# Optimization experiments

Measured on AMD Instinct MI355X. Metric: run time of the kernel, lower is better.

## Reference

```python
import jax, jax.numpy as jnp
from jax import lax
import numpy as np

B, H, Wd, CIN, COUT, KH, KW = 64, 64, 64, 128, 256, 3, 3
WSTD, BSTD = 0.3, 0.3
DN = ('NHWC', 'HWIO', 'NHWC')


def setup_inputs() -> dict:
    key = jax.random.key(0)
    k1, k2, k3, k4, k5 = jax.random.split(key, 5)
    X = jax.random.normal(k1, (B, H, Wd, CIN), dtype=jnp.float32)
    W = jax.random.normal(k2, (KH, KW, CIN, COUT), dtype=jnp.float32) * 0.05
    bias = jax.random.normal(k3, (COUT,), dtype=jnp.float32) * 0.05
    # per-sample multiplicative noise: |1 + N(0, std)| as in the original layer
    Werr = jnp.abs(1.0 + WSTD * jax.random.normal(k4, (B, KH, KW, CIN, COUT), dtype=jnp.float32))
    Berr = jnp.abs(1.0 + BSTD * jax.random.normal(k5, (B, COUT), dtype=jnp.float32))
    return {"X": X, "W": W, "bias": bias, "Werr": Werr, "Berr": Berr}


def _conv_single(x, w):
    # x: [H, W, Cin], w: [kh, kw, Cin, Cout] -> [Ho, Wo, Cout], VALID, stride 1
    return lax.conv_general_dilated(x[None], w, window_strides=(1, 1),
                                    padding='VALID', dimension_numbers=DN)[0]


def reference(X, W, bias, Werr, Berr):
    # per-sample noisy filters: memW[b] = W * Werr[b]
    memW = W[None] * Werr                        # [B, kh, kw, Cin, Cout]
    Z = jax.vmap(_conv_single)(X, memW)          # [B, Ho, Wo, Cout]
    membias = bias[None] * Berr                  # [B, Cout]
    return Z + membias[:, None, None, :]
```

## Files before the change

kernel.cpp:

```cpp
#include <hip/hip_runtime.h>
#include <hip/hip_bf16.h>

#define NB   64
#define NH   64
#define NW   64
#define NCI  128
#define NCO  256
#define NHO  62
#define NWO  62
#define MTOT (NHO*NWO)
#define KTOT (9*NCI)

#define BM  256
#define BN  256
#define BK  64
#define NKT (KTOT/BK)
#define MT  16

using bf16x8 = __attribute__((ext_vector_type(8))) short;
using f32x4  = __attribute__((ext_vector_type(4))) float;

__device__ __forceinline__ void gload_lds16(const __hip_bfloat16* g,
                                            __hip_bfloat16* l) {
    __builtin_amdgcn_global_load_lds(
        (const __attribute__((address_space(1))) unsigned int*)g,
        (__attribute__((address_space(3))) unsigned int*)l,
        16, 0, 0);
}

#define SBAR()   __builtin_amdgcn_s_barrier()
#define SCHED()  __builtin_amdgcn_sched_barrier(0)
#define VMCNT(n) asm volatile("s_waitcnt vmcnt(" #n ")" ::: "memory")

__global__ __launch_bounds__(256)
void cvt_x_kernel(const float* __restrict__ X,
                  __hip_bfloat16* __restrict__ Xb, int n8) {
    int i = blockIdx.x * 256 + threadIdx.x;
    if (i >= n8) return;
    const float4* p = (const float4*)X + (size_t)i * 2;
    float4 a = p[0], c = p[1];
    union { __hip_bfloat16 h[8]; float4 v; } u;
    u.h[0] = __float2bfloat16(a.x); u.h[1] = __float2bfloat16(a.y);
    u.h[2] = __float2bfloat16(a.z); u.h[3] = __float2bfloat16(a.w);
    u.h[4] = __float2bfloat16(c.x); u.h[5] = __float2bfloat16(c.y);
    u.h[6] = __float2bfloat16(c.z); u.h[7] = __float2bfloat16(c.w);
    *((float4*)Xb + i) = u.v;
}

#define TK 64
#define TN 64
#define TPAD 65
__global__ __launch_bounds__(256)
void build_wt_kernel(const float* __restrict__ W,
                     const float* __restrict__ Werr,
                     __hip_bfloat16* __restrict__ Wt) {
    __shared__ __hip_bfloat16 tile[TK * TPAD];
    const int t  = threadIdx.x;
    const int b  = blockIdx.z;
    const int k0 = blockIdx.x * TK;
    const int n0 = blockIdx.y * TN;

    const int c4 = (t & 15) * 4;
    const int r  = t >> 4;
    const float* wb = W + n0;
    const float* eb = Werr + (size_t)b * (KTOT * NCO) + n0;
#pragma unroll
    for (int p = 0; p < 4; p++) {
        int k  = k0 + r + p * 16;
        int kl = r + p * 16;
        float4 w = *(const float4*)(wb + (size_t)k * NCO + c4);
        float4 e = *(const float4*)(eb + (size_t)k * NCO + c4);
        tile[kl * TPAD + c4 + 0] = __float2bfloat16(w.x * e.x);
        tile[kl * TPAD + c4 + 1] = __float2bfloat16(w.y * e.y);
        tile[kl * TPAD + c4 + 2] = __float2bfloat16(w.z * e.z);
        tile[kl * TPAD + c4 + 3] = __float2bfloat16(w.w * e.w);
    }
    __syncthreads();
    const int np = t >> 2;
    const int ks = (t & 3) * 16;
    __hip_bfloat16* ob = Wt + ((size_t)b * NCO + n0 + np) * KTOT + k0 + ks;
    union { __hip_bfloat16 h[8]; float4 v; } u;
#pragma unroll
    for (int h2 = 0; h2 < 2; h2++) {
#pragma unroll
        for (int q = 0; q < 8; q++) u.h[q] = tile[(ks + h2 * 8 + q) * TPAD + np];
        *(float4*)(ob + h2 * 8) = u.v;
    }
}

__global__ __launch_bounds__(512, 2)
void gemm_bf16_kernel(const __hip_bfloat16* __restrict__ Xb,
                      const __hip_bfloat16* __restrict__ Wt,
                      const float* __restrict__ bias,
                      const float* __restrict__ Berr,
                      float* __restrict__ out) {
    __shared__ __hip_bfloat16 lds[2][2][BM * BK];

    const int t    = threadIdx.x;
    const int lane = t & 63;
    const int wave = t >> 6;

    const int bid = blockIdx.x;
    const int swz = (bid & 7) * ((NB * MT) / 8) + (bid >> 3);
    const int b   = swz >> 4;
    const int m0  = (swz & 15) * BM;

    const __hip_bfloat16* xbase = Xb + (size_t)b * (NH * NW * NCI);
    const __hip_bfloat16* wbase = Wt + (size_t)b * NCO * KTOT;

    const int srow  = t >> 3;
    const int gslot = (t & 7) ^ (srow & 7);

    int aoffg[4], boffg[4];
#pragma unroll
    for (int l = 0; l < 4; l++) {
        int row = l * 64 + srow;
        int m = m0 + row; if (m > MTOT - 1) m = MTOT - 1;
        int oh = m / NWO, ow = m - oh * NWO;
        aoffg[l] = (oh * NW + ow) * NCI + gslot * 8;
        boffg[l] = row * KTOT + gslot * 8;
    }

    auto STAGE = [&](int buf, int kt) {
        const int k0 = kt * BK;
        const int kh = k0 / (3 * NCI);
        const int rm = k0 - kh * (3 * NCI);
        const int kw = rm / NCI;
        const int ci = rm - kw * NCI;
        const int kuA = (kh * NW + kw) * NCI + ci;
        __hip_bfloat16* lA = &lds[buf][0][wave * 512];
        __hip_bfloat16* lB = &lds[buf][1][wave * 512];
#pragma unroll
        for (int l = 0; l < 4; l++) {
            gload_lds16(xbase + aoffg[l] + kuA, lA + l * 4096);
            gload_lds16(wbase + boffg[l] + k0,  lB + l * 4096);
        }
    };

    const int lrow = lane & 15, quad = lane >> 4;
    const int wm = wave >> 2;
    const int wn = wave & 3;
    const int fswz = (lrow & 7) << 3;

    f32x4 acc[8][4];
#pragma unroll
    for (int i = 0; i < 8; i++)
#pragma unroll
        for (int j = 0; j < 4; j++) acc[i][j] = (f32x4){0.f, 0.f, 0.f, 0.f};

    auto PHASE = [&](int buf, int kk) {
        const __hip_bfloat16* A  = &lds[buf][0][0];
        const __hip_bfloat16* Bp = &lds[buf][1][0];
        const int ks = (kk * 32 + quad * 8) ^ fswz;
        bf16x8 af[8], bf[4];
#pragma unroll
        for (int i = 0; i < 8; i++)
            af[i] = *(const bf16x8*)&A[(wm * 128 + i * 16 + lrow) * BK + ks];
#pragma unroll
        for (int j = 0; j < 4; j++)
            bf[j] = *(const bf16x8*)&Bp[(wn * 64 + j * 16 + lrow) * BK + ks];
        __builtin_amdgcn_s_setprio(1);
#pragma unroll
        for (int i = 0; i < 8; i++)
#pragma unroll
            for (int j = 0; j < 4; j++)
                acc[i][j] = __builtin_amdgcn_mfma_f32_16x16x32_bf16(
                    af[i], bf[j], acc[i][j], 0, 0, 0);
        __builtin_amdgcn_s_setprio(0);
    };

    STAGE(0, 0);
    STAGE(1, 1);
    VMCNT(8); SCHED();
    SBAR(); SCHED();

    for (int s = 0; s < NKT / 2 - 1; ++s) {
        PHASE(0, 0); PHASE(0, 1);
        SCHED(); SBAR(); SCHED();
        STAGE(0, 2 * s + 2);
        VMCNT(8); SCHED();
        SBAR(); SCHED();
        PHASE(1, 0); PHASE(1, 1);
        SCHED(); SBAR(); SCHED();
        STAGE(1, 2 * s + 3);
        VMCNT(8); SCHED();
        SBAR(); SCHED();
    }
    PHASE(0, 0); PHASE(0, 1);
    VMCNT(0); SCHED();
    SBAR(); SCHED();
    PHASE(1, 0); PHASE(1, 1);

    float bv[4];
#pragma unroll
    for (int j = 0; j < 4; j++) {
        int n = wn * 64 + j * 16 + lrow;
        bv[j] = bias[n] * Berr[b * NCO + n];
    }
#pragma unroll
    for (int i = 0; i < 8; i++) {
#pragma unroll
        for (int r = 0; r < 4; r++) {
            int m = m0 + wm * 128 + i * 16 + quad * 4 + r;
            if (m < MTOT) {
                float* op = out + ((size_t)b * MTOT + m) * NCO;
#pragma unroll
                for (int j = 0; j < 4; j++)
                    op[wn * 64 + j * 16 + lrow] = acc[i][j][r] + bv[j];
            }
        }
    }
}

__global__ void naive_conv_kernel(const float* __restrict__ X,
                                  const float* __restrict__ W,
                                  const float* __restrict__ bias,
                                  const float* __restrict__ Werr,
                                  const float* __restrict__ Berr,
                                  float* __restrict__ out) {
    size_t idx = (size_t)blockIdx.x * 256 + threadIdx.x;
    if (idx >= (size_t)NB * MTOT * NCO) return;
    int n = idx % NCO;
    size_t m = idx / NCO;
    int ow = m % NWO; size_t t2 = m / NWO;
    int oh = t2 % NHO; int b = t2 / NHO;
    float acc = bias[n] * Berr[b * NCO + n];
    for (int kh = 0; kh < 3; kh++)
        for (int kw = 0; kw < 3; kw++) {
            const float* xp = X + (((size_t)b * NH + oh + kh) * NW + ow + kw) * NCI;
            const float* wp = W + ((kh * 3 + kw) * NCI) * (size_t)NCO + n;
            const float* ep = Werr + (size_t)b * KTOT * NCO + ((kh * 3 + kw) * NCI) * (size_t)NCO + n;
            for (int ci = 0; ci < NCI; ci++)
                acc += xp[ci] * wp[ci * NCO] * ep[ci * NCO];
        }
    out[idx] = acc;
}

extern "C" void kernel_launch(void* const* d_in, const int* in_sizes, int n_in,
                              void* d_out, int out_size, void* d_ws, size_t ws_size,
                              hipStream_t stream) {
    const float* X    = (const float*)d_in[0];
    const float* W    = (const float*)d_in[1];
    const float* bias = (const float*)d_in[2];
    const float* Werr = (const float*)d_in[3];
    const float* Berr = (const float*)d_in[4];
    float* out = (float*)d_out;

    const size_t xb_bytes = (size_t)NB * NH * NW * NCI * 2;
    const size_t wt_bytes = (size_t)NB * NCO * KTOT * 2;

    if (ws_size < xb_bytes + wt_bytes) {
        size_t total = (size_t)NB * MTOT * NCO;
        naive_conv_kernel<<<(int)((total + 255) / 256), 256, 0, stream>>>(
            X, W, bias, Werr, Berr, out);
        return;
    }

    __hip_bfloat16* Xb = (__hip_bfloat16*)d_ws;
    __hip_bfloat16* Wt = (__hip_bfloat16*)((char*)d_ws + xb_bytes);

    int n8 = NB * NH * NW * NCI / 8;
    cvt_x_kernel<<<n8 / 256, 256, 0, stream>>>(X, Xb, n8);
    build_wt_kernel<<<dim3(KTOT / TK, NCO / TN, NB), 256, 0, stream>>>(W, Werr, Wt);
    gemm_bf16_kernel<<<dim3(NB * MT), 512, 0, stream>>>(
        Xb, Wt, bias, Berr, out);
}
```

Measured before the change: 533.7 us.

## Split MFMA main loop into four quadrant phases with barrier-paced LDS reads

```diff
diff --git a/kernel.cpp b/kernel.cpp
--- a/kernel.cpp
+++ b/kernel.cpp
@@ -31,6 +31,7 @@
 #define SBAR()   __builtin_amdgcn_s_barrier()
 #define SCHED()  __builtin_amdgcn_sched_barrier(0)
 #define VMCNT(n) asm volatile("s_waitcnt vmcnt(" #n ")" ::: "memory")
+#define LGKM0()  asm volatile("s_waitcnt lgkmcnt(0)" ::: "memory")
 
 __global__ __launch_bounds__(256)
 void cvt_x_kernel(const float* __restrict__ X,
@@ -121,15 +122,15 @@
         boffg[l] = row * KTOT + gslot * 8;
     }
 
-    auto STAGE = [&](int buf, int kt) {
+    auto STAGE = [&](int buf_, int kt) {
         const int k0 = kt * BK;
         const int kh = k0 / (3 * NCI);
         const int rm = k0 - kh * (3 * NCI);
         const int kw = rm / NCI;
         const int ci = rm - kw * NCI;
         const int kuA = (kh * NW + kw) * NCI + ci;
-        __hip_bfloat16* lA = &lds[buf][0][wave * 512];
-        __hip_bfloat16* lB = &lds[buf][1][wave * 512];
+        __hip_bfloat16* lA = &lds[buf_][0][wave * 512];
+        __hip_bfloat16* lB = &lds[buf_][1][wave * 512];
 #pragma unroll
         for (int l = 0; l < 4; l++) {
             gload_lds16(xbase + aoffg[l] + kuA, lA + l * 4096);
@@ -148,48 +149,83 @@
 #pragma unroll
         for (int j = 0; j < 4; j++) acc[i][j] = (f32x4){0.f, 0.f, 0.f, 0.f};
 
-    auto PHASE = [&](int buf, int kk) {
-        const __hip_bfloat16* A  = &lds[buf][0][0];
-        const __hip_bfloat16* Bp = &lds[buf][1][0];
-        const int ks = (kk * 32 + quad * 8) ^ fswz;
-        bf16x8 af[8], bf[4];
-#pragma unroll
-        for (int i = 0; i < 8; i++)
-            af[i] = *(const bf16x8*)&A[(wm * 128 + i * 16 + lrow) * BK + ks];
-#pragma unroll
-        for (int j = 0; j < 4; j++)
-            bf[j] = *(const bf16x8*)&Bp[(wn * 64 + j * 16 + lrow) * BK + ks];
-        __builtin_amdgcn_s_setprio(1);
-#pragma unroll
-        for (int i = 0; i < 8; i++)
-#pragma unroll
-            for (int j = 0; j < 4; j++)
-                acc[i][j] = __builtin_amdgcn_mfma_f32_16x16x32_bf16(
-                    af[i], bf[j], acc[i][j], 0, 0, 0);
-        __builtin_amdgcn_s_setprio(0);
-    };
+    bf16x8 af[4][2], bf0[2][2], bf1[2][2];
+
+#define LDA_H(IH) do {                                                         \
+    const __hip_bfloat16* Ab = &lds[buf][0][0];                                \
+    _Pragma("unroll") for (int i2 = 0; i2 < 4; i2++)                           \
+    _Pragma("unroll") for (int kh = 0; kh < 2; kh++)                           \
+        af[i2][kh] = *(const bf16x8*)&Ab[                                      \
+            (wm * 128 + ((IH) * 4 + i2) * 16 + lrow) * BK +                    \
+            ((kh * 32 + quad * 8) ^ fswz)];                                    \
+} while (0)
+
+#define LDB_H(JH, BFR) do {                                                    \
+    const __hip_bfloat16* Bb = &lds[buf][1][0];                                \
+    _Pragma("unroll") for (int j2 = 0; j2 < 2; j2++)                           \
+    _Pragma("unroll") for (int kh = 0; kh < 2; kh++)                           \
+        BFR[j2][kh] = *(const bf16x8*)&Bb[                                     \
+            (wn * 64 + ((JH) * 2 + j2) * 16 + lrow) * BK +                     \
+            ((kh * 32 + quad * 8) ^ fswz)];                                    \
+} while (0)
+
+#define MM_Q(IH, JH, BFR) do {                                                 \
+    __builtin_amdgcn_s_setprio(1);                                             \
+    _Pragma("unroll") for (int i2 = 0; i2 < 4; i2++)                           \
+    _Pragma("unroll") for (int j2 = 0; j2 < 2; j2++)                           \
+    _Pragma("unroll") for (int kh = 0; kh < 2; kh++)                           \
+        acc[(IH) * 4 + i2][(JH) * 2 + j2] =                                    \
+            __builtin_amdgcn_mfma_f32_16x16x32_bf16(                           \
+                af[i2][kh], BFR[j2][kh],                                       \
+                acc[(IH) * 4 + i2][(JH) * 2 + j2], 0, 0, 0);                   \
+    __builtin_amdgcn_s_setprio(0);                                             \
+} while (0)
+
+#define PH_WAIT() do { SCHED(); SBAR(); LGKM0(); SCHED(); } while (0)
+#define PH_BAR()  do { SCHED(); SBAR(); SCHED(); } while (0)
 
     STAGE(0, 0);
     STAGE(1, 1);
     VMCNT(8); SCHED();
     SBAR(); SCHED();
 
-    for (int s = 0; s < NKT / 2 - 1; ++s) {
-        PHASE(0, 0); PHASE(0, 1);
-        SCHED(); SBAR(); SCHED();
-        STAGE(0, 2 * s + 2);
-        VMCNT(8); SCHED();
-        SBAR(); SCHED();
-        PHASE(1, 0); PHASE(1, 1);
-        SCHED(); SBAR(); SCHED();
-        STAGE(1, 2 * s + 3);
-        VMCNT(8); SCHED();
-        SBAR(); SCHED();
-    }
-    PHASE(0, 0); PHASE(0, 1);
-    VMCNT(0); SCHED();
-    SBAR(); SCHED();
-    PHASE(1, 0); PHASE(1, 1);
+    int buf = 0;
+    for (int kt = 0; kt < NKT - 2; ++kt) {
+        LDA_H(0); LDB_H(0, bf0);
+        PH_WAIT();
+        MM_Q(0, 0, bf0);
+        PH_BAR();
+        LDB_H(1, bf1);
+        PH_WAIT();
+        MM_Q(0, 1, bf1);
+        PH_BAR();
+        LDA_H(1);
+        PH_WAIT();
+        MM_Q(1, 1, bf1);
+        PH_BAR();
+        STAGE(buf, kt + 2);
+        MM_Q(1, 0, bf0);
+        SCHED(); VMCNT(8);
+        PH_BAR();
+        buf ^= 1;
+    }
+    LDA_H(0); LDB_H(0, bf0); PH_WAIT(); MM_Q(0, 0, bf0); PH_BAR();
+    LDB_H(1, bf1);           PH_WAIT(); MM_Q(0, 1, bf1); PH_BAR();
+    LDA_H(1);                PH_WAIT(); MM_Q(1, 1, bf1); PH_BAR();
+    MM_Q(1, 0, bf0);
+    SCHED(); VMCNT(0);
+    PH_BAR();
+    buf ^= 1;
+    LDA_H(0); LDB_H(0, bf0); PH_WAIT(); MM_Q(0, 0, bf0); PH_BAR();
+    LDB_H(1, bf1);           PH_WAIT(); MM_Q(0, 1, bf1); PH_BAR();
+    LDA_H(1);                PH_WAIT(); MM_Q(1, 1, bf1); PH_BAR();
+    MM_Q(1, 0, bf0);
+
+#undef LDA_H
+#undef LDB_H
+#undef MM_Q
+#undef PH_WAIT
+#undef PH_BAR
 
     float bv[4];
 #pragma unroll
```

Result: no change. 539.1 us (+1.0%).
